# Performance work log

Measured on AMD Instinct MI355X. Metric: run time of the kernel, lower is better.

Reference implementation:

```python
import jax, jax.numpy as jnp
import numpy as np

B = 16384      # batch
D_IN = 512     # layer_channels[0]
D = 1024       # hidden width (layer_channels[1..4])
R = 16         # num_relations
SCALE = 0.02


def setup_inputs() -> dict:
    key = jax.random.key(0)
    ks = jax.random.split(key, 8)
    return {
        "x": jax.random.normal(ks[0], (B, D_IN), dtype=jnp.float32),
        "relations": jax.random.randint(ks[1], (B,), 0, R, dtype=jnp.int32),
        # non-relation dense stack (2 layers)
        "W0": jax.random.normal(ks[2], (D_IN, D), dtype=jnp.float32) * SCALE,
        "b0": jnp.zeros((D,), dtype=jnp.float32),
        "W1": jax.random.normal(ks[3], (D, D), dtype=jnp.float32) * SCALE,
        "b1": jnp.zeros((D,), dtype=jnp.float32),
        # relation-aware layers (3 layers due to the module's range(i, num_layers))
        "RW1": jax.random.normal(ks[4], (R, D, D), dtype=jnp.float32) * SCALE,
        "Rb1": jnp.zeros((R, D), dtype=jnp.float32),
        "RW2": jax.random.normal(ks[5], (R, D, D), dtype=jnp.float32) * SCALE,
        "Rb2": jnp.zeros((R, D), dtype=jnp.float32),
        "RW3": jax.random.normal(ks[6], (R, D, D), dtype=jnp.float32) * SCALE,
        "Rb3": jnp.zeros((R, D), dtype=jnp.float32),
    }


def _relation_linear(h, W, b, relations):
    """Per-sample weight selection: out[n] = h[n] @ W[rel[n]] + b[rel[n]].
    Computed as R masked GEMMs to avoid materializing per-sample [B,D,D] weights.
    """
    out = jnp.zeros((h.shape[0], W.shape[2]), dtype=h.dtype)
    for r in range(W.shape[0]):  # fixed small expert set -> ok to unroll
        mask = (relations == r)[:, None]
        out = out + jnp.where(mask, h @ W[r] + b[r], jnp.zeros((), h.dtype))
    return out


def reference(x, relations, W0, b0, W1, b1, RW1, Rb1, RW2, Rb2, RW3, Rb3):
    # non_relation_pred: Linear -> ReLU -> (dropout=identity), twice
    h = jax.nn.relu(x @ W0 + b0)
    h = jax.nn.relu(h @ W1 + b1)
    # relation layers: relu+dropout between, none after last; bn disabled
    h = jax.nn.relu(_relation_linear(h, RW1, Rb1, relations))
    h = jax.nn.relu(_relation_linear(h, RW2, Rb2, relations))
    h = _relation_linear(h, RW3, Rb3, relations)
    return h
```

## Files before the change

### kernel.cpp

```cpp
#include <hip/hip_runtime.h>
#include <stdint.h>

#define B_ROWS   16384
#define D_IN     512
#define N_DIM    1024
#define NREL     16
#define TM       128
#define TN       128
#define BK       32
#define MAX_TILES 144
#define PADDED_ROWS (MAX_TILES * TM)

typedef __bf16 bf16x8 __attribute__((ext_vector_type(8)));
typedef float  f32x4  __attribute__((ext_vector_type(4)));

__device__ __forceinline__ uint16_t f2bf(float f) {
  union { float f; uint32_t u; } v; v.f = f;
  return (uint16_t)((v.u + 0x7fffu + ((v.u >> 16) & 1u)) >> 16);
}

__device__ __forceinline__ void async_cp16(const uint16_t* g, uint16_t* l) {
  __builtin_amdgcn_global_load_lds(
      (__attribute__((address_space(1))) void*)(g),
      (__attribute__((address_space(3))) void*)(l), 16, 0, 0);
}

__global__ void setup_kernel(const int* __restrict__ rel, int* __restrict__ rowidx,
                             int* __restrict__ texp, int* __restrict__ tval) {
  __shared__ int cnt[NREL], segstart[NREL], cursor[NREL];
  const int t = threadIdx.x;
  const int nt_ = blockDim.x;
  if (t < NREL) { cnt[t] = 0; cursor[t] = 0; }
  __syncthreads();
  for (int i = t; i < B_ROWS; i += nt_) atomicAdd(&cnt[rel[i]], 1);
  __syncthreads();
  if (t == 0) {
    int slot = 0, tile = 0;
    for (int r = 0; r < NREL; r++) {
      segstart[r] = slot;
      const int c = cnt[r];
      const int nt = (c + TM - 1) / TM;
      for (int k = 0; k < nt; k++) {
        texp[tile + k] = r;
        const int rem = c - k * TM;
        tval[tile + k] = rem < TM ? rem : TM;
      }
      tile += nt; slot += nt * TM;
    }
    for (; tile < MAX_TILES; tile++) { texp[tile] = 0; tval[tile] = 0; }
  }
  __syncthreads();
  for (int i = t; i < PADDED_ROWS; i += nt_) rowidx[i] = 0;
  __syncthreads();
  for (int i = t; i < B_ROWS; i += nt_) {
    const int r = rel[i];
    const int p = atomicAdd(&cursor[r], 1);
    rowidx[segstart[r] + p] = i;
  }
}

__global__ void conv_x_kernel(const float* __restrict__ in, uint16_t* __restrict__ out, int n4) {
  const int i = blockIdx.x * blockDim.x + threadIdx.x;
  if (i < n4) {
    const float4 v = ((const float4*)in)[i];
    uint2 o;
    o.x = (uint32_t)f2bf(v.x) | ((uint32_t)f2bf(v.y) << 16);
    o.y = (uint32_t)f2bf(v.z) | ((uint32_t)f2bf(v.w) << 16);
    ((uint2*)out)[i] = o;
  }
}

__global__ __launch_bounds__(256)
void transpose_conv_kernel(const float* __restrict__ W, uint16_t* __restrict__ Wt,
                           int K, int N) {
  __shared__ uint32_t t32[64][33];
  const size_t mat = (size_t)K * N;
  const float*    Wp  = W  + mat * blockIdx.z;
  uint16_t*       Wtp = Wt + mat * blockIdx.z;
  const int n0 = blockIdx.x * 64, k0 = blockIdx.y * 64;
  const int tx = threadIdx.x & 15;
  const int ty = threadIdx.x >> 4;
  #pragma unroll
  for (int rb = 0; rb < 2; rb++) {
    const int kp = rb * 16 + ty;
    const int k  = k0 + kp * 2;
    const float4 r0 = *(const float4*)&Wp[(size_t)k * N + n0 + tx * 4];
    const float4 r1 = *(const float4*)&Wp[(size_t)(k + 1) * N + n0 + tx * 4];
    t32[tx * 4 + 0][kp] = (uint32_t)f2bf(r0.x) | ((uint32_t)f2bf(r1.x) << 16);
    t32[tx * 4 + 1][kp] = (uint32_t)f2bf(r0.y) | ((uint32_t)f2bf(r1.y) << 16);
    t32[tx * 4 + 2][kp] = (uint32_t)f2bf(r0.z) | ((uint32_t)f2bf(r1.z) << 16);
    t32[tx * 4 + 3][kp] = (uint32_t)f2bf(r0.w) | ((uint32_t)f2bf(r1.w) << 16);
  }
  __syncthreads();
  #pragma unroll
  for (int rb = 0; rb < 4; rb++) {
    const int nl = rb * 16 + ty;
    uint2 v; v.x = t32[nl][2 * tx]; v.y = t32[nl][2 * tx + 1];
    *(uint2*)&Wtp[(size_t)(n0 + nl) * K + k0 + tx * 4] = v;
  }
}

template<bool GATHER, bool EXPERT, bool RELU, bool SCATTER>
__global__ __launch_bounds__(256)
void gemm_kernel(const uint16_t* __restrict__ A, const uint16_t* __restrict__ W,
                 const float* __restrict__ bias, void* __restrict__ outp,
                 const int* __restrict__ rowidx, const int* __restrict__ texp,
                 const int* __restrict__ tval, int K) {
  __shared__ uint16_t smem[4 * TM * BK];
  uint16_t (*sA)[TM * BK] = (uint16_t (*)[TM * BK])smem;
  uint16_t (*sB)[TN * BK] = (uint16_t (*)[TN * BK])(smem + 2 * TM * BK);

  const int tid = threadIdx.x;
  const int w = tid >> 6, l = tid & 63;

  const int lin = blockIdx.x;
  const int xcd = lin & 7;
  const int j   = lin >> 3;
  const int mpx = gridDim.x >> 6;
  const int my  = xcd * mpx + (j >> 3);
  const int nx  = j & 7;
  const int m0 = my * TM;
  const int n0 = nx * TN;

  int e = 0, valid = TM;
  if (EXPERT) {
    e = texp[my];
    valid = tval[my];
    if (valid == 0) return;
  }

  const int row0   = 16 * w + (l >> 2);
  const int sel    = (row0 ^ (row0 >> 2)) & 3;
  const int koff   = ((l & 3) ^ sel) * 8;
  int ar0 = m0 + row0, ar1 = m0 + 64 + row0;
  if (GATHER) { ar0 = rowidx[ar0]; ar1 = rowidx[ar1]; }
  const uint16_t* srcA0 = A + (size_t)ar0 * K + koff;
  const uint16_t* srcA1 = A + (size_t)ar1 * K + koff;
  const uint16_t* Wb    = W + (size_t)e * N_DIM * K;
  const uint16_t* srcB0 = Wb + (size_t)(n0 + row0) * K + koff;
  const uint16_t* srcB1 = Wb + (size_t)(n0 + 64 + row0) * K + koff;
  uint16_t* ldsA0 = &sA[0][w * 512 + l * 8];
  uint16_t* ldsA1 = &sA[0][2048 + w * 512 + l * 8];
  uint16_t* ldsB0 = &sB[0][w * 512 + l * 8];
  uint16_t* ldsB1 = &sB[0][2048 + w * 512 + l * 8];

  const int wm = w >> 1, wn = w & 1;
  const int q = l >> 4, r16 = l & 15;
  const int selr = (r16 ^ (r16 >> 2)) & 3;
  const int cq = (q ^ selr) * 8;

  f32x4 acc[4][4];
  #pragma unroll
  for (int i = 0; i < 4; i++)
    #pragma unroll
    for (int jj = 0; jj < 4; jj++) {
      f32x4 z = {0.f, 0.f, 0.f, 0.f};
      acc[i][jj] = z;
    }

  const int nIter = K / BK;

  async_cp16(srcA0, ldsA0);
  async_cp16(srcA1, ldsA1);
  async_cp16(srcB0, ldsB0);
  async_cp16(srcB1, ldsB1);

  for (int k = 0; k < nIter; k++) {
    const int cur = k & 1;
    if (k + 1 < nIter) {
      const int koff2 = (k + 1) * BK;
      const int boff  = (cur ^ 1) * 4096;
      async_cp16(srcA0 + koff2, ldsA0 + boff);
      async_cp16(srcA1 + koff2, ldsA1 + boff);
      async_cp16(srcB0 + koff2, ldsB0 + boff);
      async_cp16(srcB1 + koff2, ldsB1 + boff);
      asm volatile("s_waitcnt vmcnt(4)" ::: "memory");
    } else {
      asm volatile("s_waitcnt vmcnt(0)" ::: "memory");
    }
    __builtin_amdgcn_s_barrier();

    bf16x8 af[4], bf[4];
    #pragma unroll
    for (int i = 0; i < 4; i++) {
      af[i] = *(const bf16x8*)(&sA[cur][(wm * 64 + i * 16 + r16) * BK + cq]);
      bf[i] = *(const bf16x8*)(&sB[cur][(wn * 64 + i * 16 + r16) * BK + cq]);
    }
    #pragma unroll
    for (int i = 0; i < 4; i++)
      #pragma unroll
      for (int jj = 0; jj < 4; jj++)
        acc[i][jj] = __builtin_amdgcn_mfma_f32_16x16x32_bf16(af[i], bf[jj], acc[i][jj], 0, 0, 0);

    __builtin_amdgcn_s_barrier();
  }

  float bj[4];
  #pragma unroll
  for (int jj = 0; jj < 4; jj++)
    bj[jj] = bias[(size_t)e * N_DIM + n0 + wn * 64 + jj * 16 + r16];

  if (!SCATTER) {
    #pragma unroll
    for (int i = 0; i < 4; i++)
      #pragma unroll
      for (int r = 0; r < 4; r++) {
        const int rl = wm * 64 + i * 16 + q * 4 + r;
        #pragma unroll
        for (int jj = 0; jj < 4; jj++) {
          float v = acc[i][jj][r] + bj[jj];
          if (RELU) v = fmaxf(v, 0.f);
          smem[rl * 128 + wn * 64 + jj * 16 + r16] = f2bf(v);
        }
      }
    __syncthreads();
    #pragma unroll
    for (int c = 0; c < 8; c++) {
      const int off16 = c * 2048 + tid * 8;
      const int row = off16 >> 7, col = off16 & 127;
      uint16_t* dst = (uint16_t*)outp + (size_t)(m0 + row) * N_DIM + n0 + col;
      *(uint4*)dst = *(const uint4*)&smem[off16];
    }
  } else {
    float* smemf = (float*)smem;
    #pragma unroll
    for (int h = 0; h < 2; h++) {
      if (h) __syncthreads();
      #pragma unroll
      for (int ii = 0; ii < 2; ii++) {
        const int i = 2 * h + ii;
        #pragma unroll
        for (int r = 0; r < 4; r++) {
          const int lr = wm * 32 + ii * 16 + q * 4 + r;
          #pragma unroll
          for (int jj = 0; jj < 4; jj++) {
            float v = acc[i][jj][r] + bj[jj];
            if (RELU) v = fmaxf(v, 0.f);
            smemf[lr * 128 + wn * 64 + jj * 16 + r16] = v;
          }
        }
      }
      __syncthreads();
      #pragma unroll
      for (int c = 0; c < 8; c++) {
        const int offB = c * 4096 + tid * 16;
        const int lr = offB >> 9, colf = (offB & 511) >> 2;
        const int wmr = lr >> 5, rem = lr & 31;
        const int rl = wmr * 64 + (2 * h + (rem >> 4)) * 16 + (rem & 15);
        if (rl < valid) {
          const int orow = rowidx[m0 + rl];
          float* dst = (float*)outp + (size_t)orow * N_DIM + n0 + colf;
          *(float4*)dst = *(const float4*)((const char*)smemf + offB);
        }
      }
    }
  }
}

extern "C" void kernel_launch(void* const* d_in, const int* in_sizes, int n_in,
                              void* d_out, int out_size, void* d_ws, size_t ws_size,
                              hipStream_t stream) {
  const float* x   = (const float*)d_in[0];
  const int*   rel = (const int*)d_in[1];
  const float* W0  = (const float*)d_in[2];
  const float* b0  = (const float*)d_in[3];
  const float* W1  = (const float*)d_in[4];
  const float* b1  = (const float*)d_in[5];
  const float* RW1 = (const float*)d_in[6];
  const float* Rb1 = (const float*)d_in[7];
  const float* RW2 = (const float*)d_in[8];
  const float* Rb2 = (const float*)d_in[9];
  const float* RW3 = (const float*)d_in[10];
  const float* Rb3 = (const float*)d_in[11];
  float* out = (float*)d_out;

  char* ws = (char*)d_ws;
  uint16_t* xb = (uint16_t*)(ws);
  uint16_t* wt = (uint16_t*)(ws + (size_t)(16u << 20));
  uint16_t* ha = (uint16_t*)(ws + (size_t)(48u << 20));
  uint16_t* hb = (uint16_t*)(ws + (size_t)(84u << 20));
  int* rowidx = (int*)(ws + (size_t)(120u << 20));
  int* texp   = rowidx + PADDED_ROWS;
  int* tval   = texp + MAX_TILES;

  const dim3 blk(256);
  const dim3 gDense(8 * (B_ROWS / TM));
  const dim3 gRel(8 * MAX_TILES);

  setup_kernel<<<dim3(1), dim3(1024), 0, stream>>>(rel, rowidx, texp, tval);
  conv_x_kernel<<<dim3((B_ROWS * D_IN) / 4 / 256), blk, 0, stream>>>(x, xb, (B_ROWS * D_IN) / 4);

  transpose_conv_kernel<<<dim3(N_DIM / 64, D_IN / 64, 1), blk, 0, stream>>>(W0, wt, D_IN, N_DIM);
  gemm_kernel<false, false, true, false><<<gDense, blk, 0, stream>>>(
      xb, wt, b0, ha, nullptr, nullptr, nullptr, D_IN);

  transpose_conv_kernel<<<dim3(N_DIM / 64, N_DIM / 64, 1), blk, 0, stream>>>(W1, wt, N_DIM, N_DIM);
  gemm_kernel<false, false, true, false><<<gDense, blk, 0, stream>>>(
      ha, wt, b1, hb, nullptr, nullptr, nullptr, N_DIM);

  transpose_conv_kernel<<<dim3(N_DIM / 64, N_DIM / 64, NREL), blk, 0, stream>>>(RW1, wt, N_DIM, N_DIM);
  gemm_kernel<true, true, true, false><<<gRel, blk, 0, stream>>>(
      hb, wt, Rb1, ha, rowidx, texp, tval, N_DIM);

  transpose_conv_kernel<<<dim3(N_DIM / 64, N_DIM / 64, NREL), blk, 0, stream>>>(RW2, wt, N_DIM, N_DIM);
  gemm_kernel<false, true, true, false><<<gRel, blk, 0, stream>>>(
      ha, wt, Rb2, hb, rowidx, texp, tval, N_DIM);

  transpose_conv_kernel<<<dim3(N_DIM / 64, N_DIM / 64, NREL), blk, 0, stream>>>(RW3, wt, N_DIM, N_DIM);
  gemm_kernel<false, true, false, true><<<gRel, blk, 0, stream>>>(
      hb, wt, Rb3, out, rowidx, texp, tval, N_DIM);

  (void)in_sizes; (void)n_in; (void)out_size; (void)ws_size;
}
```

Before: 521.0 us.

## Widen GEMM output tile to 128x256 with 4x8 MFMA fragments per wave

Doubles the N tile from 128 to 256, so each wave computes a 64x128 sub-tile with 32 accumulators. The A-tile loads and LDS reads are reused across twice as many MFMAs, cutting A traffic and the barrier count per FLOP. The block-to-tile mapping, grid sizes and epilogue staging (done in two or four passes through LDS) are rewritten to match. In exchange, accumulator register pressure doubles and the grid has half as many blocks, which may lower occupancy.

```diff
diff --git a/kernel.cpp b/kernel.cpp
--- a/kernel.cpp
+++ b/kernel.cpp
@@ -6,7 +6,7 @@
 #define N_DIM    1024
 #define NREL     16
 #define TM       128
-#define TN       128
+#define TN       256
 #define BK       32
 #define MAX_TILES 144
 #define PADDED_ROWS (MAX_TILES * TM)
@@ -106,19 +106,17 @@
                  const float* __restrict__ bias, void* __restrict__ outp,
                  const int* __restrict__ rowidx, const int* __restrict__ texp,
                  const int* __restrict__ tval, int K) {
-  __shared__ uint16_t smem[4 * TM * BK];
-  uint16_t (*sA)[TM * BK] = (uint16_t (*)[TM * BK])smem;
-  uint16_t (*sB)[TN * BK] = (uint16_t (*)[TN * BK])(smem + 2 * TM * BK);
+  __shared__ uint16_t smem[2 * TM * BK + 2 * TN * BK];
 
   const int tid = threadIdx.x;
   const int w = tid >> 6, l = tid & 63;
 
   const int lin = blockIdx.x;
   const int xcd = lin & 7;
-  const int j   = lin >> 3;
-  const int mpx = gridDim.x >> 6;
-  const int my  = xcd * mpx + (j >> 3);
-  const int nx  = j & 7;
+  const int j2  = lin >> 3;
+  const int mpx = gridDim.x >> 5;
+  const int my  = xcd * mpx + (j2 >> 2);
+  const int nx  = j2 & 3;
   const int m0 = my * TM;
   const int n0 = nx * TN;
 
@@ -137,23 +135,27 @@
   const uint16_t* srcA0 = A + (size_t)ar0 * K + koff;
   const uint16_t* srcA1 = A + (size_t)ar1 * K + koff;
   const uint16_t* Wb    = W + (size_t)e * N_DIM * K;
-  const uint16_t* srcB0 = Wb + (size_t)(n0 + row0) * K + koff;
-  const uint16_t* srcB1 = Wb + (size_t)(n0 + 64 + row0) * K + koff;
-  uint16_t* ldsA0 = &sA[0][w * 512 + l * 8];
-  uint16_t* ldsA1 = &sA[0][2048 + w * 512 + l * 8];
-  uint16_t* ldsB0 = &sB[0][w * 512 + l * 8];
-  uint16_t* ldsB1 = &sB[0][2048 + w * 512 + l * 8];
+  const uint16_t* srcB0 = Wb + (size_t)(n0 +       row0) * K + koff;
+  const uint16_t* srcB1 = Wb + (size_t)(n0 +  64 + row0) * K + koff;
+  const uint16_t* srcB2 = Wb + (size_t)(n0 + 128 + row0) * K + koff;
+  const uint16_t* srcB3 = Wb + (size_t)(n0 + 192 + row0) * K + koff;
+  uint16_t* ldsA0 = &smem[w * 512 + l * 8];
+  uint16_t* ldsA1 = ldsA0 + 2048;
+  uint16_t* ldsB0 = &smem[8192 + w * 512 + l * 8];
+  uint16_t* ldsB1 = ldsB0 + 2048;
+  uint16_t* ldsB2 = ldsB0 + 4096;
+  uint16_t* ldsB3 = ldsB0 + 6144;
 
   const int wm = w >> 1, wn = w & 1;
   const int q = l >> 4, r16 = l & 15;
   const int selr = (r16 ^ (r16 >> 2)) & 3;
   const int cq = (q ^ selr) * 8;
 
-  f32x4 acc[4][4];
+  f32x4 acc[4][8];
   #pragma unroll
   for (int i = 0; i < 4; i++)
     #pragma unroll
-    for (int jj = 0; jj < 4; jj++) {
+    for (int jj = 0; jj < 8; jj++) {
       f32x4 z = {0.f, 0.f, 0.f, 0.f};
       acc[i][jj] = z;
     }
@@ -164,93 +166,104 @@
   async_cp16(srcA1, ldsA1);
   async_cp16(srcB0, ldsB0);
   async_cp16(srcB1, ldsB1);
+  async_cp16(srcB2, ldsB2);
+  async_cp16(srcB3, ldsB3);
 
   for (int k = 0; k < nIter; k++) {
     const int cur = k & 1;
     if (k + 1 < nIter) {
-      const int koff2 = (k + 1) * BK;
-      const int boff  = (cur ^ 1) * 4096;
-      async_cp16(srcA0 + koff2, ldsA0 + boff);
-      async_cp16(srcA1 + koff2, ldsA1 + boff);
-      async_cp16(srcB0 + koff2, ldsB0 + boff);
-      async_cp16(srcB1 + koff2, ldsB1 + boff);
-      asm volatile("s_waitcnt vmcnt(4)" ::: "memory");
+      const int ko   = (k + 1) * BK;
+      const int aoff = (cur ^ 1) * 4096;
+      const int boff = (cur ^ 1) * 8192;
+      async_cp16(srcA0 + ko, ldsA0 + aoff);
+      async_cp16(srcA1 + ko, ldsA1 + aoff);
+      async_cp16(srcB0 + ko, ldsB0 + boff);
+      async_cp16(srcB1 + ko, ldsB1 + boff);
+      async_cp16(srcB2 + ko, ldsB2 + boff);
+      async_cp16(srcB3 + ko, ldsB3 + boff);
+      asm volatile("s_waitcnt vmcnt(6)" ::: "memory");
     } else {
       asm volatile("s_waitcnt vmcnt(0)" ::: "memory");
     }
     __builtin_amdgcn_s_barrier();
 
-    bf16x8 af[4], bf[4];
-    #pragma unroll
-    for (int i = 0; i < 4; i++) {
-      af[i] = *(const bf16x8*)(&sA[cur][(wm * 64 + i * 16 + r16) * BK + cq]);
-      bf[i] = *(const bf16x8*)(&sB[cur][(wn * 64 + i * 16 + r16) * BK + cq]);
-    }
+    bf16x8 af[4], bf[8];
+    const uint16_t* bA = &smem[cur * 4096];
+    const uint16_t* bB = &smem[8192 + cur * 8192];
     #pragma unroll
     for (int i = 0; i < 4; i++)
-      #pragma unroll
-      for (int jj = 0; jj < 4; jj++)
+      af[i] = *(const bf16x8*)(&bA[(wm * 64 + i * 16 + r16) * BK + cq]);
+    #pragma unroll
+    for (int jj = 0; jj < 8; jj++)
+      bf[jj] = *(const bf16x8*)(&bB[(wn * 128 + jj * 16 + r16) * BK + cq]);
+    #pragma unroll
+    for (int i = 0; i < 4; i++)
+      #pragma unroll
+      for (int jj = 0; jj < 8; jj++)
         acc[i][jj] = __builtin_amdgcn_mfma_f32_16x16x32_bf16(af[i], bf[jj], acc[i][jj], 0, 0, 0);
 
     __builtin_amdgcn_s_barrier();
   }
 
-  float bj[4];
+  float bj[8];
   #pragma unroll
-  for (int jj = 0; jj < 4; jj++)
-    bj[jj] = bias[(size_t)e * N_DIM + n0 + wn * 64 + jj * 16 + r16];
+  for (int jj = 0; jj < 8; jj++)
+    bj[jj] = bias[(size_t)e * N_DIM + n0 + wn * 128 + jj * 16 + r16];
 
   if (!SCATTER) {
     #pragma unroll
-    for (int i = 0; i < 4; i++)
-      #pragma unroll
-      for (int r = 0; r < 4; r++) {
-        const int rl = wm * 64 + i * 16 + q * 4 + r;
+    for (int h = 0; h < 2; h++) {
+      if (h) __syncthreads();
+      #pragma unroll
+      for (int i = 0; i < 4; i++)
         #pragma unroll
-        for (int jj = 0; jj < 4; jj++) {
-          float v = acc[i][jj][r] + bj[jj];
-          if (RELU) v = fmaxf(v, 0.f);
-          smem[rl * 128 + wn * 64 + jj * 16 + r16] = f2bf(v);
+        for (int r = 0; r < 4; r++) {
+          const int rl = wm * 64 + i * 16 + q * 4 + r;
+          #pragma unroll
+          for (int jj = 0; jj < 4; jj++) {
+            float v = acc[i][4 * h + jj][r] + bj[4 * h + jj];
+            if (RELU) v = fmaxf(v, 0.f);
+            smem[rl * 128 + wn * 64 + jj * 16 + r16] = f2bf(v);
+          }
         }
+      __syncthreads();
+      #pragma unroll
+      for (int c = 0; c < 8; c++) {
+        const int off16 = c * 2048 + tid * 8;
+        const int row = off16 >> 7, colp = off16 & 127;
+        const int gcol = n0 + (colp >> 6) * 128 + h * 64 + (colp & 63);
+        uint16_t* dst = (uint16_t*)outp + (size_t)(m0 + row) * N_DIM + gcol;
+        *(uint4*)dst = *(const uint4*)&smem[off16];
       }
-    __syncthreads();
-    #pragma unroll
-    for (int c = 0; c < 8; c++) {
-      const int off16 = c * 2048 + tid * 8;
-      const int row = off16 >> 7, col = off16 & 127;
-      uint16_t* dst = (uint16_t*)outp + (size_t)(m0 + row) * N_DIM + n0 + col;
-      *(uint4*)dst = *(const uint4*)&smem[off16];
     }
   } else {
     float* smemf = (float*)smem;
     #pragma unroll
-    for (int h = 0; h < 2; h++) {
+    for (int h = 0; h < 4; h++) {
       if (h) __syncthreads();
       #pragma unroll
-      for (int ii = 0; ii < 2; ii++) {
-        const int i = 2 * h + ii;
+      for (int i = 0; i < 4; i++)
         #pragma unroll
         for (int r = 0; r < 4; r++) {
-          const int lr = wm * 32 + ii * 16 + q * 4 + r;
+          const int rl = wm * 64 + i * 16 + q * 4 + r;
           #pragma unroll
-          for (int jj = 0; jj < 4; jj++) {
-            float v = acc[i][jj][r] + bj[jj];
+          for (int jj = 0; jj < 2; jj++) {
+            float v = acc[i][2 * h + jj][r] + bj[2 * h + jj];
             if (RELU) v = fmaxf(v, 0.f);
-            smemf[lr * 128 + wn * 64 + jj * 16 + r16] = v;
+            smemf[rl * 64 + wn * 32 + jj * 16 + r16] = v;
           }
         }
-      }
       __syncthreads();
       #pragma unroll
       for (int c = 0; c < 8; c++) {
         const int offB = c * 4096 + tid * 16;
-        const int lr = offB >> 9, colf = (offB & 511) >> 2;
-        const int wmr = lr >> 5, rem = lr & 31;
-        const int rl = wmr * 64 + (2 * h + (rem >> 4)) * 16 + (rem & 15);
-        if (rl < valid) {
-          const int orow = rowidx[m0 + rl];
-          float* dst = (float*)outp + (size_t)orow * N_DIM + n0 + colf;
-          *(float4*)dst = *(const float4*)((const char*)smemf + offB);
+        const int row = offB >> 8;
+        const int colp = (offB & 255) >> 2;
+        if (row < valid) {
+          const int orow = EXPERT ? rowidx[m0 + row] : (m0 + row);
+          const int gcol = (colp >> 5) * 128 + h * 32 + (colp & 31);
+          float* dst = (float*)outp + (size_t)orow * N_DIM + n0 + gcol;
+          *(float4*)dst = *(const float4*)&smemf[offB >> 2];
         }
       }
     }
@@ -284,8 +297,8 @@
   int* tval   = texp + MAX_TILES;
 
   const dim3 blk(256);
-  const dim3 gDense(8 * (B_ROWS / TM));
-  const dim3 gRel(8 * MAX_TILES);
+  const dim3 gDense((B_ROWS / TM) * (N_DIM / TN));
+  const dim3 gRel(MAX_TILES * (N_DIM / TN));
 
   setup_kernel<<<dim3(1), dim3(1024), 0, stream>>>(rel, rowidx, texp, tval);
   conv_x_kernel<<<dim3((B_ROWS * D_IN) / 4 / 256), blk, 0, stream>>>(x, xb, (B_ROWS * D_IN) / 4);
```

Result: slower. 571.3 us (+9.7%).
